# Optimization experiments

Hardware: AMD Instinct MI355X
Metric: run time of the kernel (lower is better)

## Reference

```python
import jax, jax.numpy as jnp
import numpy as np

N = 50000      # nodes
E = 800000     # edges (avg degree 16)
IN = 128       # input feature dim
D = 128        # embed dim (heads=1, concat)
SLOPE = 0.2    # GATv2Conv default negative_slope


def setup_inputs() -> dict:
    key = jax.random.key(0)
    ks = jax.random.split(key, 16)
    s_in = 1.0 / np.sqrt(IN)
    s_d = 1.0 / np.sqrt(D)
    inp = {
        "node_fts": jax.random.normal(ks[0], (N, IN), dtype=jnp.float32),
        "edge_index": jax.random.randint(ks[1], (2, E), 0, N, dtype=jnp.int64),
        # layer 1 (in_dim -> embed_dim)
        "Wl1": jax.random.normal(ks[2], (IN, D), dtype=jnp.float32) * s_in,
        "bl1": jnp.zeros((D,), dtype=jnp.float32),
        "Wr1": jax.random.normal(ks[3], (IN, D), dtype=jnp.float32) * s_in,
        "br1": jnp.zeros((D,), dtype=jnp.float32),
        "att1": jax.random.normal(ks[4], (D,), dtype=jnp.float32) * s_d,
        "bias1": jnp.zeros((D,), dtype=jnp.float32),
        # layer 2 (embed_dim -> embed_dim)
        "Wl2": jax.random.normal(ks[5], (D, D), dtype=jnp.float32) * s_d,
        "bl2": jnp.zeros((D,), dtype=jnp.float32),
        "Wr2": jax.random.normal(ks[6], (D, D), dtype=jnp.float32) * s_d,
        "br2": jnp.zeros((D,), dtype=jnp.float32),
        "att2": jax.random.normal(ks[7], (D,), dtype=jnp.float32) * s_d,
        "bias2": jnp.zeros((D,), dtype=jnp.float32),
    }
    return inp


def gatv2_layer(x, src, dst, Wl, bl, Wr, br, att, bias):
    # GATv2Conv (heads=1, share_weights=False):
    #   x_j (source message features) = lin_l(x), x_i (target) = lin_r(x)
    xl = x @ Wl + bl                                      # [N, D]
    xr = x @ Wr + br                                      # [N, D]
    e = jax.nn.leaky_relu(xl[src] + xr[dst], SLOPE)       # [E, D]
    logits = e @ att                                      # [E]
    # softmax over incoming edges of each target node
    m = jax.ops.segment_max(logits, dst, num_segments=N)  # [N], -inf for isolated
    m = jnp.where(jnp.isneginf(m), 0.0, m)
    a = jnp.exp(logits - m[dst])                          # [E]
    s = jax.ops.segment_sum(a, dst, num_segments=N)       # [N]
    a = a / jnp.maximum(s[dst], 1e-16)
    out = jax.ops.segment_sum(a[:, None] * xl[src], dst, num_segments=N)  # [N, D]
    return out + bias


def reference(node_fts, edge_index,
              Wl1, bl1, Wr1, br1, att1, bias1,
              Wl2, bl2, Wr2, br2, att2, bias2):
    src, dst = edge_index[0], edge_index[1]
    x = jax.nn.relu(gatv2_layer(node_fts, src, dst, Wl1, bl1, Wr1, br1, att1, bias1))
    x = jax.nn.relu(gatv2_layer(x, src, dst, Wl2, bl2, Wr2, br2, att2, bias2))
    return x
```

## Files before the change

### kernel.cpp

```cpp
#include <hip/hip_runtime.h>
#include <hip/hip_bf16.h>
#include <hip/hip_fp16.h>

#define N_NODES 50000
#define N_EDGES 800000
#define DIM 128
#define NGROUPS (N_NODES / 16)
#define LROW2 132
#define KBUCKET 196
#define BCAP 5120
#define EPB 2000
#define NSLOT (KBUCKET*256)

typedef __attribute__((ext_vector_type(8))) _Float16 hfrag8;
typedef __attribute__((ext_vector_type(4))) float f32x4;
typedef _Float16 h2 __attribute__((ext_vector_type(2)));

__device__ __forceinline__ h2 u2h(uint u){ union{uint u; h2 h;} c; c.u = u; return c.h; }

__device__ __forceinline__ float rowsum16(float p) {
  union { float f; int i; } a, b;
  a.f = p;
  b.i = __builtin_amdgcn_update_dpp(0, a.i, 0x128, 0xF, 0xF, true); a.f += b.f;
  b.i = __builtin_amdgcn_update_dpp(0, a.i, 0x124, 0xF, 0xF, true); a.f += b.f;
  b.i = __builtin_amdgcn_update_dpp(0, a.i, 0x122, 0xF, 0xF, true); a.f += b.f;
  b.i = __builtin_amdgcn_update_dpp(0, a.i, 0x121, 0xF, 0xF, true); a.f += b.f;
  return a.f;
}


__global__ __launch_bounds__(256) void bucket_scatter_k(
    const int* __restrict__ src, const int* __restrict__ dst,
    int* __restrict__ bucket_cnt, uint* __restrict__ bucketdata)
{
  __shared__ int cnt[KBUCKET], base[KBUCKET], cur[KBUCKET];
  int tid = threadIdx.x;
  for (int t = tid; t < KBUCKET; t += 256) { cnt[t] = 0; cur[t] = 0; }
  __syncthreads();
  int e0 = blockIdx.x * EPB;
  int dreg[8];
  #pragma unroll
  for (int it = 0; it < 8; it++) {
    int i = it*256 + tid;
    dreg[it] = (i < EPB) ? dst[e0 + i] : -1;
    if (i < EPB) atomicAdd(&cnt[dreg[it] >> 8], 1);
  }
  __syncthreads();
  for (int t = tid; t < KBUCKET; t += 256)
    base[t] = atomicAdd(&bucket_cnt[t], cnt[t]);
  __syncthreads();
  #pragma unroll
  for (int it = 0; it < 8; it++) {
    int i = it*256 + tid;
    if (i < EPB) {
      int s = src[e0 + i], d = dreg[it];
      int b = d >> 8;
      int r = atomicAdd(&cur[b], 1);
      bucketdata[(size_t)b * BCAP + base[b] + r] = ((uint)s << 8) | (uint)(d & 255);
    }
  }
}

__global__ __launch_bounds__(64) void prep_w(
    const float* __restrict__ Wl1, const float* __restrict__ Wr1,
    const float* __restrict__ Wl2, const float* __restrict__ Wr2,
    _Float16* __restrict__ wb, int* __restrict__ bucket_cnt)
{
  int bid = blockIdx.x;
  if (bid == 0) {
    for (int t = threadIdx.x; t < KBUCKET; t += 64) bucket_cnt[t] = 0;
  }
  int layer = bid >> 6, rest = bid & 63;
  int C = rest >> 4, g = rest & 15;
  int lane = threadIdx.x;
  int m = lane & 15, q = lane >> 4;
  int dim = g*16 + m;
  const float* W = layer ? (dim < 128 ? Wl2 : Wr2) : (dim < 128 ? Wl1 : Wr1);
  int dcol = dim & 127;
  _Float16 h[8];
  #pragma unroll
  for (int j = 0; j < 8; j++) {
    int k = C*32 + q*8 + j;
    h[j] = (_Float16)W[(size_t)k*DIM + dcol];
  }
  size_t off = ((size_t)bid*64 + lane)*8;
  *(hfrag8*)(wb + off) = *(hfrag8*)h;
}

__global__ __launch_bounds__(256) void gemm1_csr_k(
    const float* __restrict__ x, const _Float16* __restrict__ wb,
    const float* __restrict__ bl, const float* __restrict__ br,
    __half* __restrict__ xlh, __half* __restrict__ xrh,
    const int* __restrict__ bucket_cnt, const uint* __restrict__ bucketdata,
    int* __restrict__ row_start, int* __restrict__ csr_soff,
    int* __restrict__ perm)
{
  __shared__ float lds[4][16*LROW2];
  __shared__ int hist[256], cur[256];
  __shared__ int wsumA[4], wsumB[4];
  __shared__ int dhist[64], dbase[64], dcur[64];
  int tid = threadIdx.x;

  if (blockIdx.x < KBUCKET) {
    int b = blockIdx.x;
    int lane = tid & 63, w = tid >> 6;
    int vv = (tid < b) ? bucket_cnt[tid] : 0;
    #pragma unroll
    for (int off = 32; off > 0; off >>= 1) vv += __shfl_xor(vv, off, 64);
    if (lane == 0) wsumA[w] = vv;
    hist[tid] = 0;
    if (tid < 64) { dhist[tid] = 0; dcur[tid] = 0; }
    __syncthreads();
    int base_csr = wsumA[0] + wsumA[1] + wsumA[2] + wsumA[3];
    int cnt = bucket_cnt[b];
    int node0 = b << 8;
    const uint* bd = bucketdata + (size_t)b * BCAP;
    for (int i = tid; i < cnt; i += 256)
      atomicAdd(&hist[bd[i] & 255], 1);
    __syncthreads();
    int v = hist[tid];
    int node = node0 + tid;
    int degc = (node < N_NODES) ? min(v, 63) : 63;
    atomicAdd(&dhist[degc], 1);
    int inc = v;
    #pragma unroll
    for (int off = 1; off < 64; off <<= 1) {
      int y = __shfl_up(inc, off, 64);
      if (lane >= off) inc += y;
    }
    if (lane == 63) wsumB[w] = inc;
    __syncthreads();
    int wpre = 0;
    #pragma unroll
    for (int i = 0; i < 4; i++) if (i < w) wpre += wsumB[i];
    int excl = wpre + inc - v;
    if (node < N_NODES) row_start[node] = base_csr + excl;
    if (b == 0 && tid == 0) row_start[N_NODES] = N_EDGES;
    cur[tid] = excl;
    if (tid < 64) {
      int c = dhist[tid];
      int ic = c;
      #pragma unroll
      for (int off = 1; off < 64; off <<= 1) {
        int y = __shfl_up(ic, off, 64);
        if (tid >= off) ic += y;
      }
      dbase[tid] = ic - c;
    }
    __syncthreads();
    int rank = dbase[degc] + atomicAdd(&dcur[degc], 1);
    perm[node0 + rank] = node;
    for (int i = tid; i < cnt; i += 256) {
      uint p = bd[i];
      int r = atomicAdd(&cur[p & 255], 1);
      csr_soff[base_csr + r] = (int)(p & 0xFFFFFF00u);
    }
    return;
  }

  int wv = tid >> 6, lane = tid & 63;
  int G = (blockIdx.x - KBUCKET) * 4 + wv;
  if (G >= NGROUPS) return;

  int m = lane & 15, q = lane >> 4;
  const float* xrow = x + (size_t)(G*16 + m)*DIM + q*8;

  f32x4 acc[16];
  #pragma unroll
  for (int g = 0; g < 16; g++) acc[g] = (f32x4)(0.f);

  #pragma unroll 1
  for (int C = 0; C < 4; C++) {
    float v[8];
    *(float4*)(v)     = *(const float4*)(xrow + C*32);
    *(float4*)(v + 4) = *(const float4*)(xrow + C*32 + 4);
    _Float16 hh[8];
    #pragma unroll
    for (int j = 0; j < 8; j++) hh[j] = (_Float16)v[j];
    hfrag8 ah = *(hfrag8*)hh;
    #pragma unroll
    for (int g = 0; g < 16; g++) {
      size_t boff = ((size_t)(C*16 + g)*64 + lane)*8;
      hfrag8 bh = *(const hfrag8*)(wb + boff);
      acc[g] = __builtin_amdgcn_mfma_f32_16x16x32_f16(ah, bh, acc[g], 0, 0, 0);
    }
  }

  float* wlds = lds[wv];
  int dcol = (lane & 31) * 4;
  int rowsel = lane >> 5;
  #pragma unroll
  for (int half = 0; half < 2; half++) {
    #pragma unroll
    for (int g = 0; g < 8; g++) {
      #pragma unroll
      for (int r = 0; r < 4; r++)
        wlds[(q*4 + r)*LROW2 + g*16 + m] = acc[half*8 + g][r];
    }
    const float* B = half ? br : bl;
    ushort* outh = half ? (ushort*)xrh : (ushort*)xlh;
    float4 bv = *(const float4*)(B + dcol);
    #pragma unroll
    for (int it = 0; it < 8; it++) {
      int i = it*2 + rowsel;
      float4 vv2 = *(const float4*)(wlds + i*LROW2 + dcol);
      int node = G*16 + i;
      __half2 h0 = __floats2half2_rn(vv2.x + bv.x, vv2.y + bv.y);
      __half2 h1 = __floats2half2_rn(vv2.z + bv.z, vv2.w + bv.w);
      uint2 pk = make_uint2(*(uint*)&h0, *(uint*)&h1);
      *(uint2*)(outh + (size_t)node*DIM + dcol) = pk;
    }
  }
}


#define GAT_LDI(OFF, TBASE)                                             \
  _Pragma("unroll")                                                     \
  for (int j = 0; j < 4; j++) {                                         \
    int rr = r0 + (TBASE) + j;                                          \
    OFF[j] = csr_soff[rr <= last ? rr : last];                          \
  }

#define GAT_LDR(OFF, RAW)                                               \
  _Pragma("unroll")                                                     \
  for (int j = 0; j < 4; j++)                                           \
    RAW[j] = *(const uint4*)(xb + (size_t)(uint)OFF[j]);

#define GAT_COMP(RAW, TBASE)                                            \
  _Pragma("unroll")                                                     \
  for (int j = 0; j < 4; j++) {                                         \
    h2 v01 = u2h(RAW[j].x), v23 = u2h(RAW[j].y);                        \
    h2 v45 = u2h(RAW[j].z), v67 = u2h(RAW[j].w);                        \
    h2 s01 = v01 + xr01, s23 = v23 + xr23;                              \
    h2 s45 = v45 + xr45, s67 = v67 + xr67;                              \
    s01 = __builtin_elementwise_max(s01, s01 * c02);                    \
    s23 = __builtin_elementwise_max(s23, s23 * c02);                    \
    s45 = __builtin_elementwise_max(s45, s45 * c02);                    \
    s67 = __builtin_elementwise_max(s67, s67 * c02);                    \
    float pA = __builtin_amdgcn_fdot2(s01, a01, 0.f, false);            \
    pA = __builtin_amdgcn_fdot2(s23, a23, pA, false);                   \
    float pB = __builtin_amdgcn_fdot2(s45, a45, 0.f, false);            \
    pB = __builtin_amdgcn_fdot2(s67, a67, pB, false);                   \
    float p = rowsum16(pA + pB);                                        \
    float w = ((TBASE) + j < deg) ? __expf(p) : 0.f;                    \
    l += w;                                                             \
    b0a = fmaf(w, (float)v01.x, b0a); b1a = fmaf(w, (float)v01.y, b1a); \
    b2a = fmaf(w, (float)v23.x, b2a); b3a = fmaf(w, (float)v23.y, b3a); \
    b4a = fmaf(w, (float)v45.x, b4a); b5a = fmaf(w, (float)v45.y, b5a); \
    b6a = fmaf(w, (float)v67.x, b6a); b7a = fmaf(w, (float)v67.y, b7a); \
  }

__device__ __forceinline__ void gather_core(
    int node, int valid, int hl,
    const __half* __restrict__ xlh, const __half* __restrict__ xrh,
    const int* __restrict__ row_start, const int* __restrict__ csr_soff,
    const float* __restrict__ att, const float* __restrict__ bias,
    float4& o0, float4& o1)
{
  int r0 = row_start[node];
  int deg = row_start[node + 1] - r0;
  if (!valid) deg = 0;
  int last = r0 + deg - 1;

  uint4 rx = *(const uint4*)((const ushort*)xrh + (size_t)node*DIM + hl*8);
  h2 xr01 = u2h(rx.x), xr23 = u2h(rx.y), xr45 = u2h(rx.z), xr67 = u2h(rx.w);
  const float* ap = att + hl*8;
  float4 af0 = *(const float4*)(ap);
  float4 af1 = *(const float4*)(ap + 4);
  h2 a01 = {(_Float16)af0.x, (_Float16)af0.y};
  h2 a23 = {(_Float16)af0.z, (_Float16)af0.w};
  h2 a45 = {(_Float16)af1.x, (_Float16)af1.y};
  h2 a67 = {(_Float16)af1.z, (_Float16)af1.w};
  const h2 c02 = {(_Float16)0.2f, (_Float16)0.2f};

  float l = 0.f;
  float b0a=0,b1a=0,b2a=0,b3a=0,b4a=0,b5a=0,b6a=0,b7a=0;
  const char* xb = (const char*)xlh + hl*16;

  int offA[4]; uint4 rawA[4];
  int offB[4]; uint4 rawB[4];

  if (deg > 0) { GAT_LDI(offA, 0); GAT_LDR(offA, rawA); }
  for (int t = 0; t < deg; t += 8) {
    bool hasB = (t + 4 < deg);
    if (hasB) { GAT_LDI(offB, t + 4); GAT_LDR(offB, rawB); }
    GAT_COMP(rawA, t);
    if (t + 8 < deg) { GAT_LDI(offA, t + 8); GAT_LDR(offA, rawA); }
    if (hasB) GAT_COMP(rawB, t + 4);
  }

  float inv = 1.f / fmaxf(l, 1e-16f);
  const float* bp = bias + hl*8;
  float4 c0 = *(const float4*)(bp);
  float4 c1 = *(const float4*)(bp + 4);
  o0.x = fmaxf(fmaf(b0a, inv, c0.x), 0.f);
  o0.y = fmaxf(fmaf(b1a, inv, c0.y), 0.f);
  o0.z = fmaxf(fmaf(b2a, inv, c0.z), 0.f);
  o0.w = fmaxf(fmaf(b3a, inv, c0.w), 0.f);
  o1.x = fmaxf(fmaf(b4a, inv, c1.x), 0.f);
  o1.y = fmaxf(fmaf(b5a, inv, c1.y), 0.f);
  o1.z = fmaxf(fmaf(b6a, inv, c1.z), 0.f);
  o1.w = fmaxf(fmaf(b7a, inv, c1.w), 0.f);
}

__global__ __launch_bounds__(256) void fused_g1_gemm2_k(
    const __half* __restrict__ xlh, const __half* __restrict__ xrh,
    const int* __restrict__ row_start, const int* __restrict__ csr_soff,
    const int* __restrict__ perm,
    const float* __restrict__ att, const float* __restrict__ bias,
    const _Float16* __restrict__ wb2,
    const float* __restrict__ bl2, const float* __restrict__ br2,
    __half* __restrict__ xlh2, __half* __restrict__ xrh2)
{
  __shared__ ushort xs[16*128];
  __shared__ ushort outs[16*256];
  __shared__ int nodes_s[16];
  int tid = threadIdx.x;
  int wv = tid >> 6, lane = tid & 63;
  int q4 = lane >> 4, hl = lane & 15;
  int nl = wv*4 + q4;
  int base = blockIdx.x * 16;

  int node = perm[base + nl];
  int valid = node < N_NODES;
  int nodec = valid ? node : 0;
  if (hl == 0) nodes_s[nl] = node;
  float4 o0, o1;
  gather_core(nodec, valid, hl, xlh, xrh, row_start, csr_soff, att, bias, o0, o1);
  __half2 p0 = __floats2half2_rn(o0.x, o0.y);
  __half2 p1 = __floats2half2_rn(o0.z, o0.w);
  __half2 p2 = __floats2half2_rn(o1.x, o1.y);
  __half2 p3 = __floats2half2_rn(o1.z, o1.w);
  uint4 pk = make_uint4(*(uint*)&p0, *(uint*)&p1, *(uint*)&p2, *(uint*)&p3);
  *(uint4*)((char*)xs + nl*256 + ((hl*16) ^ ((nl&7)<<4))) = pk;
  __syncthreads();

  int m = lane & 15, q = lane >> 4;
  f32x4 acc[4];
  #pragma unroll
  for (int g = 0; g < 4; g++) acc[g] = (f32x4)(0.f);
  #pragma unroll
  for (int C = 0; C < 4; C++) {
    hfrag8 ah = *(const hfrag8*)((const char*)xs + m*256 + ((C*64 + q*16) ^ ((m&7)<<4)));
    #pragma unroll
    for (int g = 0; g < 4; g++) {
      int gg = wv*4 + g;
      size_t boff = ((size_t)(C*16 + gg)*64 + lane)*8;
      hfrag8 bh = *(const hfrag8*)(wb2 + boff);
      acc[g] = __builtin_amdgcn_mfma_f32_16x16x32_f16(ah, bh, acc[g], 0, 0, 0);
    }
  }
  #pragma unroll
  for (int g = 0; g < 4; g++) {
    int gg = wv*4 + g;
    int dim = gg*16 + m;
    float bv = (gg < 8) ? bl2[dim] : br2[dim - 128];
    #pragma unroll
    for (int r = 0; r < 4; r++) {
      int row = q*4 + r;
      __half hv = __float2half_rn(acc[g][r] + bv);
      outs[row*256 + gg*16 + m] = *(ushort*)&hv;
    }
  }
  __syncthreads();
  #pragma unroll
  for (int p = 0; p < 2; p++) {
    int c = p*256 + tid;
    int row = c >> 5, off = c & 31;
    uint4 v = *(const uint4*)((const char*)outs + row*512 + off*16);
    int nodeo = nodes_s[row];
    int d0 = off*8;
    ushort* dstp = (d0 < 128) ? ((ushort*)xlh2 + (size_t)nodeo*DIM + d0)
                              : ((ushort*)xrh2 + (size_t)nodeo*DIM + (d0 - 128));
    *(uint4*)dstp = v;
  }
}

__global__ __launch_bounds__(256) void gat_gather2(
    const __half* __restrict__ xlh, const __half* __restrict__ xrh,
    const int* __restrict__ row_start, const int* __restrict__ csr_soff,
    const int* __restrict__ perm,
    const float* __restrict__ att, const float* __restrict__ bias,
    float* __restrict__ outf)
{
  int wave = (blockIdx.x * 256 + threadIdx.x) >> 6;
  int lane = threadIdx.x & 63;
  int q4 = lane >> 4;
  int hl = lane & 15;
  int slot = wave * 4 + q4;
  int node = perm[slot];
  int valid = node < N_NODES;
  int nodec = valid ? node : 0;
  float4 o0, o1;
  gather_core(nodec, valid, hl, xlh, xrh, row_start, csr_soff, att, bias, o0, o1);
  if (valid) {
    float* op = outf + (size_t)node*DIM + hl*8;
    *(float4*)(op)     = o0;
    *(float4*)(op + 4) = o1;
  }
}

extern "C" void kernel_launch(void* const* d_in, const int* in_sizes, int n_in,
                              void* d_out, int out_size, void* d_ws, size_t ws_size,
                              hipStream_t stream)
{
  const float* node_fts = (const float*)d_in[0];
  const int*  edge_index = (const int*)d_in[1];
  const float* Wl1 = (const float*)d_in[2];
  const float* bl1 = (const float*)d_in[3];
  const float* Wr1 = (const float*)d_in[4];
  const float* br1 = (const float*)d_in[5];
  const float* att1 = (const float*)d_in[6];
  const float* bias1 = (const float*)d_in[7];
  const float* Wl2 = (const float*)d_in[8];
  const float* bl2 = (const float*)d_in[9];
  const float* Wr2 = (const float*)d_in[10];
  const float* br2 = (const float*)d_in[11];
  const float* att2 = (const float*)d_in[12];
  const float* bias2 = (const float*)d_in[13];
  const int* src = edge_index;
  const int* dst = edge_index + N_EDGES;

  char* ws = (char*)d_ws;
  __half* xlh = (__half*)ws;               ws += (size_t)N_NODES*DIM*2;
  __half* xrh = (__half*)ws;               ws += (size_t)N_NODES*DIM*2;
  __half* xlh2 = (__half*)ws;              ws += (size_t)NSLOT*DIM*2;
  __half* xrh2 = (__half*)ws;              ws += (size_t)NSLOT*DIM*2;
  _Float16* wb = (_Float16*)ws;            ws += 2*4*16*64*8*2;
  int* row_start   = (int*)ws;             ws += (N_NODES+1)*4;
  int* csr_soff    = (int*)ws;             ws += (size_t)N_EDGES*4;
  int* perm        = (int*)ws;             ws += (size_t)NSLOT*4;
  int* bucket_cnt  = (int*)ws;             ws += KBUCKET*4;
  uint* bucketdata = (uint*)ws;            ws += (size_t)KBUCKET*BCAP*4;

  const int W_LAYER = 4*16*64*8;

  int gemm_blocks = (NGROUPS + 3) / 4;
  int slot_blocks = NSLOT / 16;

  prep_w<<<128, 64, 0, stream>>>(Wl1, Wr1, Wl2, Wr2, wb, bucket_cnt);
  bucket_scatter_k<<<N_EDGES/EPB, 256, 0, stream>>>(src, dst, bucket_cnt, bucketdata);
  gemm1_csr_k<<<KBUCKET + gemm_blocks, 256, 0, stream>>>(
      node_fts, wb, bl1, br1, xlh, xrh,
      bucket_cnt, bucketdata, row_start, csr_soff, perm);
  fused_g1_gemm2_k<<<slot_blocks, 256, 0, stream>>>(
      xlh, xrh, row_start, csr_soff, perm, att1, bias1,
      wb + W_LAYER, bl2, br2, xlh2, xrh2);
  gat_gather2<<<slot_blocks, 256, 0, stream>>>(
      xlh2, xrh2, row_start, csr_soff, perm, att2, bias2, (float*)d_out);
}
```

Baseline: 229.9 us.

## Drop degree-sorted node permutation and restructure gather/GEMM2 into single-wave blocks

Removes the per-bucket degree sort and perm array, so the gathers process nodes in natural order. The edge loop now handles full groups of four without clamping and a masked remainder, and uses exp2 with log2(e) folded into the attention vector. The fused layer-1 gather plus layer-2 GEMM kernel becomes one 64-thread wave per 16 nodes: it loops over four node rows, then runs the MFMA in two halves and reuses LDS for output staging. This cuts sort work, perm indirection and barriers, at the cost of losing degree-balanced waves and adding serial work per wave.

```diff
diff --git a/kernel.cpp b/kernel.cpp
--- a/kernel.cpp
+++ b/kernel.cpp
@@ -10,7 +10,6 @@
 #define KBUCKET 196
 #define BCAP 5120
 #define EPB 2000
-#define NSLOT (KBUCKET*256)
 
 typedef __attribute__((ext_vector_type(8))) _Float16 hfrag8;
 typedef __attribute__((ext_vector_type(4))) float f32x4;
@@ -92,13 +91,11 @@
     const float* __restrict__ bl, const float* __restrict__ br,
     __half* __restrict__ xlh, __half* __restrict__ xrh,
     const int* __restrict__ bucket_cnt, const uint* __restrict__ bucketdata,
-    int* __restrict__ row_start, int* __restrict__ csr_soff,
-    int* __restrict__ perm)
+    int* __restrict__ row_start, int* __restrict__ csr_soff)
 {
   __shared__ float lds[4][16*LROW2];
   __shared__ int hist[256], cur[256];
   __shared__ int wsumA[4], wsumB[4];
-  __shared__ int dhist[64], dbase[64], dcur[64];
   int tid = threadIdx.x;
 
   if (blockIdx.x < KBUCKET) {
@@ -109,7 +106,6 @@
     for (int off = 32; off > 0; off >>= 1) vv += __shfl_xor(vv, off, 64);
     if (lane == 0) wsumA[w] = vv;
     hist[tid] = 0;
-    if (tid < 64) { dhist[tid] = 0; dcur[tid] = 0; }
     __syncthreads();
     int base_csr = wsumA[0] + wsumA[1] + wsumA[2] + wsumA[3];
     int cnt = bucket_cnt[b];
@@ -119,9 +115,6 @@
       atomicAdd(&hist[bd[i] & 255], 1);
     __syncthreads();
     int v = hist[tid];
-    int node = node0 + tid;
-    int degc = (node < N_NODES) ? min(v, 63) : 63;
-    atomicAdd(&dhist[degc], 1);
     int inc = v;
     #pragma unroll
     for (int off = 1; off < 64; off <<= 1) {
@@ -134,22 +127,11 @@
     #pragma unroll
     for (int i = 0; i < 4; i++) if (i < w) wpre += wsumB[i];
     int excl = wpre + inc - v;
+    int node = node0 + tid;
     if (node < N_NODES) row_start[node] = base_csr + excl;
     if (b == 0 && tid == 0) row_start[N_NODES] = N_EDGES;
     cur[tid] = excl;
-    if (tid < 64) {
-      int c = dhist[tid];
-      int ic = c;
-      #pragma unroll
-      for (int off = 1; off < 64; off <<= 1) {
-        int y = __shfl_up(ic, off, 64);
-        if (tid >= off) ic += y;
-      }
-      dbase[tid] = ic - c;
-    }
     __syncthreads();
-    int rank = dbase[degc] + atomicAdd(&dcur[degc], 1);
-    perm[node0 + rank] = node;
     for (int i = tid; i < cnt; i += 256) {
       uint p = bd[i];
       int r = atomicAdd(&cur[p & 255], 1);
@@ -214,19 +196,16 @@
 }
 
 
-#define GAT_LDI(OFF, TBASE)                                             \
+#define GAT_LDI4(OFF, RBASE)                                            \
   _Pragma("unroll")                                                     \
-  for (int j = 0; j < 4; j++) {                                         \
-    int rr = r0 + (TBASE) + j;                                          \
-    OFF[j] = csr_soff[rr <= last ? rr : last];                          \
-  }
-
-#define GAT_LDR(OFF, RAW)                                               \
+  for (int j = 0; j < 4; j++) OFF[j] = csr_soff[(RBASE) + j];
+
+#define GAT_LDR4(OFF, RAW)                                              \
   _Pragma("unroll")                                                     \
   for (int j = 0; j < 4; j++)                                           \
     RAW[j] = *(const uint4*)(xb + (size_t)(uint)OFF[j]);
 
-#define GAT_COMP(RAW, TBASE)                                            \
+#define GAT_BODY(RAW, WEXPR)                                            \
   _Pragma("unroll")                                                     \
   for (int j = 0; j < 4; j++) {                                         \
     h2 v01 = u2h(RAW[j].x), v23 = u2h(RAW[j].y);                        \
@@ -242,7 +221,7 @@
     float pB = __builtin_amdgcn_fdot2(s45, a45, 0.f, false);            \
     pB = __builtin_amdgcn_fdot2(s67, a67, pB, false);                   \
     float p = rowsum16(pA + pB);                                        \
-    float w = ((TBASE) + j < deg) ? __expf(p) : 0.f;                    \
+    float w = (WEXPR);                                                  \
     l += w;                                                             \
     b0a = fmaf(w, (float)v01.x, b0a); b1a = fmaf(w, (float)v01.y, b1a); \
     b2a = fmaf(w, (float)v23.x, b2a); b3a = fmaf(w, (float)v23.y, b3a); \
@@ -251,7 +230,7 @@
   }
 
 __device__ __forceinline__ void gather_core(
-    int node, int valid, int hl,
+    int node, int hl,
     const __half* __restrict__ xlh, const __half* __restrict__ xrh,
     const int* __restrict__ row_start, const int* __restrict__ csr_soff,
     const float* __restrict__ att, const float* __restrict__ bias,
@@ -259,18 +238,17 @@
 {
   int r0 = row_start[node];
   int deg = row_start[node + 1] - r0;
-  if (!valid) deg = 0;
-  int last = r0 + deg - 1;
 
   uint4 rx = *(const uint4*)((const ushort*)xrh + (size_t)node*DIM + hl*8);
   h2 xr01 = u2h(rx.x), xr23 = u2h(rx.y), xr45 = u2h(rx.z), xr67 = u2h(rx.w);
   const float* ap = att + hl*8;
   float4 af0 = *(const float4*)(ap);
   float4 af1 = *(const float4*)(ap + 4);
-  h2 a01 = {(_Float16)af0.x, (_Float16)af0.y};
-  h2 a23 = {(_Float16)af0.z, (_Float16)af0.w};
-  h2 a45 = {(_Float16)af1.x, (_Float16)af1.y};
-  h2 a67 = {(_Float16)af1.z, (_Float16)af1.w};
+  const float L2E = 1.44269504088896f;
+  h2 a01 = {(_Float16)(af0.x*L2E), (_Float16)(af0.y*L2E)};
+  h2 a23 = {(_Float16)(af0.z*L2E), (_Float16)(af0.w*L2E)};
+  h2 a45 = {(_Float16)(af1.x*L2E), (_Float16)(af1.y*L2E)};
+  h2 a67 = {(_Float16)(af1.z*L2E), (_Float16)(af1.w*L2E)};
   const h2 c02 = {(_Float16)0.2f, (_Float16)0.2f};
 
   float l = 0.f;
@@ -279,14 +257,26 @@
 
   int offA[4]; uint4 rawA[4];
   int offB[4]; uint4 rawB[4];
-
-  if (deg > 0) { GAT_LDI(offA, 0); GAT_LDR(offA, rawA); }
-  for (int t = 0; t < deg; t += 8) {
-    bool hasB = (t + 4 < deg);
-    if (hasB) { GAT_LDI(offB, t + 4); GAT_LDR(offB, rawB); }
-    GAT_COMP(rawA, t);
-    if (t + 8 < deg) { GAT_LDI(offA, t + 8); GAT_LDR(offA, rawA); }
-    if (hasB) GAT_COMP(rawB, t + 4);
+  int nfull = deg & ~3;
+
+  if (nfull > 0) { GAT_LDI4(offA, r0); GAT_LDR4(offA, rawA); }
+  #pragma unroll 1
+  for (int t = 0; t < nfull; t += 8) {
+    bool hasB = (t + 4 < nfull);
+    if (hasB) { GAT_LDI4(offB, r0 + t + 4); GAT_LDR4(offB, rawB); }
+    GAT_BODY(rawA, exp2f(p));
+    if (t + 8 < nfull) { GAT_LDI4(offA, r0 + t + 8); GAT_LDR4(offA, rawA); }
+    if (hasB) GAT_BODY(rawB, exp2f(p));
+  }
+  int rem = deg - nfull;
+  if (rem > 0) {
+    #pragma unroll
+    for (int j = 0; j < 4; j++) {
+      int rr = r0 + nfull + (j < rem ? j : rem - 1);
+      offA[j] = csr_soff[rr];
+    }
+    GAT_LDR4(offA, rawA);
+    GAT_BODY(rawA, (j < rem) ? exp2f(p) : 0.f);
   }
 
   float inv = 1.f / fmaxf(l, 1e-16f);
@@ -303,83 +293,75 @@
   o1.w = fmaxf(fmaf(b7a, inv, c1.w), 0.f);
 }
 
-__global__ __launch_bounds__(256) void fused_g1_gemm2_k(
+__global__ __launch_bounds__(64, 4) void fused_g1_gemm2_k(
     const __half* __restrict__ xlh, const __half* __restrict__ xrh,
     const int* __restrict__ row_start, const int* __restrict__ csr_soff,
-    const int* __restrict__ perm,
     const float* __restrict__ att, const float* __restrict__ bias,
     const _Float16* __restrict__ wb2,
     const float* __restrict__ bl2, const float* __restrict__ br2,
     __half* __restrict__ xlh2, __half* __restrict__ xrh2)
 {
-  __shared__ ushort xs[16*128];
-  __shared__ ushort outs[16*256];
-  __shared__ int nodes_s[16];
-  int tid = threadIdx.x;
-  int wv = tid >> 6, lane = tid & 63;
+  __shared__ ushort xs[16*132];
+  int lane = threadIdx.x;
   int q4 = lane >> 4, hl = lane & 15;
-  int nl = wv*4 + q4;
   int base = blockIdx.x * 16;
 
-  int node = perm[base + nl];
-  int valid = node < N_NODES;
-  int nodec = valid ? node : 0;
-  if (hl == 0) nodes_s[nl] = node;
-  float4 o0, o1;
-  gather_core(nodec, valid, hl, xlh, xrh, row_start, csr_soff, att, bias, o0, o1);
-  __half2 p0 = __floats2half2_rn(o0.x, o0.y);
-  __half2 p1 = __floats2half2_rn(o0.z, o0.w);
-  __half2 p2 = __floats2half2_rn(o1.x, o1.y);
-  __half2 p3 = __floats2half2_rn(o1.z, o1.w);
-  uint4 pk = make_uint4(*(uint*)&p0, *(uint*)&p1, *(uint*)&p2, *(uint*)&p3);
-  *(uint4*)((char*)xs + nl*256 + ((hl*16) ^ ((nl&7)<<4))) = pk;
-  __syncthreads();
-
-  int m = lane & 15, q = lane >> 4;
-  f32x4 acc[4];
-  #pragma unroll
-  for (int g = 0; g < 4; g++) acc[g] = (f32x4)(0.f);
-  #pragma unroll
-  for (int C = 0; C < 4; C++) {
-    hfrag8 ah = *(const hfrag8*)((const char*)xs + m*256 + ((C*64 + q*16) ^ ((m&7)<<4)));
-    #pragma unroll
-    for (int g = 0; g < 4; g++) {
-      int gg = wv*4 + g;
-      size_t boff = ((size_t)(C*16 + gg)*64 + lane)*8;
-      hfrag8 bh = *(const hfrag8*)(wb2 + boff);
-      acc[g] = __builtin_amdgcn_mfma_f32_16x16x32_f16(ah, bh, acc[g], 0, 0, 0);
-    }
-  }
-  #pragma unroll
-  for (int g = 0; g < 4; g++) {
-    int gg = wv*4 + g;
-    int dim = gg*16 + m;
-    float bv = (gg < 8) ? bl2[dim] : br2[dim - 128];
-    #pragma unroll
-    for (int r = 0; r < 4; r++) {
-      int row = q*4 + r;
-      __half hv = __float2half_rn(acc[g][r] + bv);
-      outs[row*256 + gg*16 + m] = *(ushort*)&hv;
-    }
-  }
-  __syncthreads();
-  #pragma unroll
-  for (int p = 0; p < 2; p++) {
-    int c = p*256 + tid;
-    int row = c >> 5, off = c & 31;
-    uint4 v = *(const uint4*)((const char*)outs + row*512 + off*16);
-    int nodeo = nodes_s[row];
-    int d0 = off*8;
-    ushort* dstp = (d0 < 128) ? ((ushort*)xlh2 + (size_t)nodeo*DIM + d0)
-                              : ((ushort*)xrh2 + (size_t)nodeo*DIM + (d0 - 128));
-    *(uint4*)dstp = v;
+  #pragma unroll 1
+  for (int rr = 0; rr < 4; rr++) {
+    int nl = rr*4 + q4;
+    float4 o0, o1;
+    gather_core(base + nl, hl, xlh, xrh, row_start, csr_soff, att, bias, o0, o1);
+    __half2 p0 = __floats2half2_rn(o0.x, o0.y);
+    __half2 p1 = __floats2half2_rn(o0.z, o0.w);
+    __half2 p2 = __floats2half2_rn(o1.x, o1.y);
+    __half2 p3 = __floats2half2_rn(o1.z, o1.w);
+    uint4 pk = make_uint4(*(uint*)&p0, *(uint*)&p1, *(uint*)&p2, *(uint*)&p3);
+    *(uint4*)((char*)xs + nl*264 + ((hl*16) ^ ((nl&7)<<4))) = pk;
+  }
+
+  hfrag8 ah[4];
+  #pragma unroll
+  for (int C = 0; C < 4; C++)
+    ah[C] = *(const hfrag8*)((const char*)xs + hl*264 +
+                             ((C*64 + q4*16) ^ ((hl&7)<<4)));
+
+  #pragma unroll 1
+  for (int half = 0; half < 2; half++) {
+    f32x4 acc[8];
+    #pragma unroll
+    for (int g = 0; g < 8; g++) acc[g] = (f32x4)(0.f);
+    #pragma unroll
+    for (int C = 0; C < 4; C++) {
+      #pragma unroll
+      for (int g = 0; g < 8; g++) {
+        int gg = half*8 + g;
+        hfrag8 bh = *(const hfrag8*)(wb2 + ((size_t)(C*16 + gg)*64 + lane)*8);
+        acc[g] = __builtin_amdgcn_mfma_f32_16x16x32_f16(ah[C], bh, acc[g], 0, 0, 0);
+      }
+    }
+    const float* B = half ? br2 : bl2;
+    #pragma unroll
+    for (int g = 0; g < 8; g++) {
+      float bv = B[g*16 + hl];
+      #pragma unroll
+      for (int r = 0; r < 4; r++) {
+        __half hv = __float2half_rn(acc[g][r] + bv);
+        xs[(q4*4 + r)*132 + g*16 + hl] = *(ushort*)&hv;
+      }
+    }
+    __half* dsth = half ? xrh2 : xlh2;
+    #pragma unroll
+    for (int i = 0; i < 4; i++) {
+      int row = i*4 + q4;
+      uint4 v = *(const uint4*)((const char*)xs + row*264 + hl*16);
+      *(uint4*)((ushort*)dsth + (size_t)(base + row)*DIM + hl*8) = v;
+    }
   }
 }
 
 __global__ __launch_bounds__(256) void gat_gather2(
     const __half* __restrict__ xlh, const __half* __restrict__ xrh,
     const int* __restrict__ row_start, const int* __restrict__ csr_soff,
-    const int* __restrict__ perm,
     const float* __restrict__ att, const float* __restrict__ bias,
     float* __restrict__ outf)
 {
@@ -387,17 +369,12 @@
   int lane = threadIdx.x & 63;
   int q4 = lane >> 4;
   int hl = lane & 15;
-  int slot = wave * 4 + q4;
-  int node = perm[slot];
-  int valid = node < N_NODES;
-  int nodec = valid ? node : 0;
+  int node = wave * 4 + q4;
   float4 o0, o1;
-  gather_core(nodec, valid, hl, xlh, xrh, row_start, csr_soff, att, bias, o0, o1);
-  if (valid) {
-    float* op = outf + (size_t)node*DIM + hl*8;
-    *(float4*)(op)     = o0;
-    *(float4*)(op + 4) = o1;
-  }
+  gather_core(node, hl, xlh, xrh, row_start, csr_soff, att, bias, o0, o1);
+  float* op = outf + (size_t)node*DIM + hl*8;
+  *(float4*)(op)     = o0;
+  *(float4*)(op + 4) = o1;
 }
 
 extern "C" void kernel_launch(void* const* d_in, const int* in_sizes, int n_in,
@@ -424,28 +401,27 @@
   char* ws = (char*)d_ws;
   __half* xlh = (__half*)ws;               ws += (size_t)N_NODES*DIM*2;
   __half* xrh = (__half*)ws;               ws += (size_t)N_NODES*DIM*2;
-  __half* xlh2 = (__half*)ws;              ws += (size_t)NSLOT*DIM*2;
-  __half* xrh2 = (__half*)ws;              ws += (size_t)NSLOT*DIM*2;
+  __half* xlh2 = (__half*)ws;              ws += (size_t)N_NODES*DIM*2;
+  __half* xrh2 = (__half*)ws;              ws += (size_t)N_NODES*DIM*2;
   _Float16* wb = (_Float16*)ws;            ws += 2*4*16*64*8*2;
   int* row_start   = (int*)ws;             ws += (N_NODES+1)*4;
   int* csr_soff    = (int*)ws;             ws += (size_t)N_EDGES*4;
-  int* perm        = (int*)ws;             ws += (size_t)NSLOT*4;
   int* bucket_cnt  = (int*)ws;             ws += KBUCKET*4;
   uint* bucketdata = (uint*)ws;            ws += (size_t)KBUCKET*BCAP*4;
 
   const int W_LAYER = 4*16*64*8;
 
   int gemm_blocks = (NGROUPS + 3) / 4;
-  int slot_blocks = NSLOT / 16;
+  int gather_blocks = N_NODES / 16;
 
   prep_w<<<128, 64, 0, stream>>>(Wl1, Wr1, Wl2, Wr2, wb, bucket_cnt);
   bucket_scatter_k<<<N_EDGES/EPB, 256, 0, stream>>>(src, dst, bucket_cnt, bucketdata);
   gemm1_csr_k<<<KBUCKET + gemm_blocks, 256, 0, stream>>>(
       node_fts, wb, bl1, br1, xlh, xrh,
-      bucket_cnt, bucketdata, row_start, csr_soff, perm);
-  fused_g1_gemm2_k<<<slot_blocks, 256, 0, stream>>>(
-      xlh, xrh, row_start, csr_soff, perm, att1, bias1,
+      bucket_cnt, bucketdata, row_start, csr_soff);
+  fused_g1_gemm2_k<<<NGROUPS, 64, 0, stream>>>(
+      xlh, xrh, row_start, csr_soff, att1, bias1,
       wb + W_LAYER, bl2, br2, xlh2, xrh2);
-  gat_gather2<<<slot_blocks, 256, 0, stream>>>(
-      xlh2, xrh2, row_start, csr_soff, perm, att2, bias2, (float*)d_out);
-}
+  gat_gather2<<<gather_blocks, 256, 0, stream>>>(
+      xlh2, xrh2, row_start, csr_soff, att2, bias2, (float*)d_out);
+}
```

New measurement: 228.8 us. No clear change (-0.5%).
